# Optimization experiments

Measured on AMD Instinct MI355X. Metric: run time of the kernel, lower is better.

## Reference

```python
import jax, jax.numpy as jnp
import numpy as np

K = 3
STRIDE = 1
PAD = 1


def _conv(x, w, b):
    y = jax.lax.conv_general_dilated(
        x, w, window_strides=(STRIDE, STRIDE),
        padding=[(PAD, PAD), (PAD, PAD)],
        dimension_numbers=('NCHW', 'OIHW', 'NCHW'))
    return y + b[None, :, None, None]


def setup_inputs() -> dict:
    key = jax.random.key(0)
    ks = jax.random.split(key, 6)
    B, Cin, H, W = 4, 64, 128, 128
    Cout = 128
    x = jax.random.normal(ks[0], (B, Cin, H, W), dtype=jnp.float32)
    # small random offset/mask conv params (original inits to 0, which would be degenerate)
    w_off = jax.random.normal(ks[1], (2 * K * K, Cin, K, K), dtype=jnp.float32) * 0.01
    b_off = jax.random.normal(ks[2], (2 * K * K,), dtype=jnp.float32) * 0.1
    w_mask = jax.random.normal(ks[3], (K * K, Cin, K, K), dtype=jnp.float32) * 0.01
    b_mask = jnp.zeros((K * K,), dtype=jnp.float32)
    # kaiming_uniform(a=sqrt(5)) -> bound = 1/sqrt(fan_in)
    fan_in = Cin * K * K
    bound = 1.0 / np.sqrt(fan_in)
    weight = jax.random.uniform(ks[4], (Cout, Cin, K, K), dtype=jnp.float32,
                                minval=-bound, maxval=bound)
    return {"x": x, "w_off": w_off, "b_off": b_off,
            "w_mask": w_mask, "b_mask": b_mask, "weight": weight}


def _deform_conv(x, offset, mask, weight):
    B, C, H, W = x.shape
    O = weight.shape[0]
    KK = K * K
    Ho, Wo = offset.shape[2], offset.shape[3]
    # torchvision layout: offset[:, 2k] = dy_k, offset[:, 2k+1] = dx_k
    off = offset.reshape(B, KK, 2, Ho, Wo)
    dy, dx = off[:, :, 0], off[:, :, 1]  # [B,KK,Ho,Wo]

    ky, kx = jnp.meshgrid(jnp.arange(K), jnp.arange(K), indexing='ij')
    ky = ky.reshape(KK).astype(jnp.float32)
    kx = kx.reshape(KK).astype(jnp.float32)
    oy = jnp.arange(Ho, dtype=jnp.float32) * STRIDE - PAD
    ox = jnp.arange(Wo, dtype=jnp.float32) * STRIDE - PAD
    # sampling positions [B,KK,Ho,Wo]
    py = oy[None, None, :, None] + ky[None, :, None, None] + dy
    px = ox[None, None, None, :] + kx[None, :, None, None] + dx

    y0 = jnp.floor(py)
    x0 = jnp.floor(px)
    ly = py - y0
    lx = px - x0
    y0i = y0.astype(jnp.int32)
    x0i = x0.astype(jnp.int32)

    x_flat = x.reshape(B, C, H * W)
    gather = jax.vmap(lambda xf, idx: xf[:, idx])  # ([C,HW],[KK,Ho,Wo])->[C,KK,Ho,Wo]

    def corner(yi, xi, wgt):
        valid = ((yi >= 0) & (yi < H) & (xi >= 0) & (xi < W)).astype(x.dtype)
        yc = jnp.clip(yi, 0, H - 1)
        xc = jnp.clip(xi, 0, W - 1)
        g = gather(x_flat, yc * W + xc)  # [B,C,KK,Ho,Wo]
        return g * (wgt * valid)[:, None]

    sampled = (corner(y0i, x0i, (1 - ly) * (1 - lx))
               + corner(y0i, x0i + 1, (1 - ly) * lx)
               + corner(y0i + 1, x0i, ly * (1 - lx))
               + corner(y0i + 1, x0i + 1, ly * lx))  # [B,C,KK,Ho,Wo]

    sampled = sampled * mask[:, None]  # modulation, mask [B,KK,Ho,Wo]
    w = weight.reshape(O, C, KK)
    return jnp.einsum('bckhw,ock->bohw', sampled, w)


def reference(x, w_off, b_off, w_mask, b_mask, weight):
    offset = _conv(x, w_off, b_off)
    mask = jax.nn.sigmoid(_conv(x, w_mask, b_mask))
    return _deform_conv(x, offset, mask, weight)
```

## Files before the change

kernel.cpp:

```cpp
#include <hip/hip_runtime.h>
#include <math.h>

#define B 4
#define CIN 64
#define H 128
#define W 128
#define COUT 128
#define KK 9
#define HW (H*W)

#define WBF_COLS 640
#define WBF_SHORTS (COUT*WBF_COLS)
#define WCV_SHORTS (32*640)
#define LDK 168

typedef __attribute__((ext_vector_type(8))) short short8;
typedef __attribute__((ext_vector_type(4))) float f32x4;
typedef __attribute__((ext_vector_type(2))) float f32x2;
typedef f32x2 __attribute__((aligned(4))) f32x2a;

#define GLDS16(g, l) __builtin_amdgcn_global_load_lds(                        \
    (__attribute__((address_space(1))) void*)(g),                             \
    (__attribute__((address_space(3))) void*)(l), 16, 0, 0)

__device__ __forceinline__ unsigned short f2bf(float f) {
    unsigned int u = __float_as_uint(f);
    u += 0x7fffu + ((u >> 16) & 1u);
    return (unsigned short)(u >> 16);
}

__global__ void prep_all(const float* __restrict__ wgt,
                         const float* __restrict__ w_off, const float* __restrict__ b_off,
                         const float* __restrict__ w_mask, const float* __restrict__ b_mask,
                         short* __restrict__ wbf, short* __restrict__ wcv,
                         float* __restrict__ bcat)
{
    int idx = blockIdx.x * 256 + threadIdx.x;
    if (idx < WBF_SHORTS) {
        int o  = idx / WBF_COLS;
        int kp = idx % WBF_COLS;
        int cb = kp / 160, r = kp % 160;
        float v = 0.f;
        if (r < 144) {
            int tap = r >> 4;
            int c   = cb * 16 + (r & 15);
            v = wgt[(o * CIN + c) * KK + tap];
        }
        wbf[idx] = (short)f2bf(v);
    } else {
        int j = idx - WBF_SHORTS;
        if (j < WCV_SHORTS) {
            int f  = j / 640;
            int kp = j % 640;
            int cb = kp / 160, r = kp % 160;
            float v = 0.f;
            if (r < 144) {
                int tap = r >> 4;
                int c   = cb * 16 + (r & 15);
                if (f < 18)      v = w_off[(f * CIN + c) * 9 + tap];
                else if (f < 27) v = w_mask[((f - 18) * CIN + c) * 9 + tap];
            }
            wcv[j] = (short)f2bf(v);
        }
        if (blockIdx.x == WBF_SHORTS / 256 && threadIdx.x < 32) {
            int f = threadIdx.x;
            float bv = 0.f;
            if (f < 18) bv = b_off[f];
            else if (f < 27) bv = b_mask[f - 18];
            bcat[f] = bv;
        }
    }
}

__global__ __launch_bounds__(256, 2) void fused4_kernel(
    const float* __restrict__ x, const short* __restrict__ wcv,
    const short* __restrict__ wbf, const float* __restrict__ bcat,
    float* __restrict__ out)
{
    const int bid = blockIdx.x;
    const int T = (bid & 7) * 128 + (bid >> 3);
    const int wo0 = (T & 1) * 64;
    const int ho  = (T >> 1) & 127;
    const int b   = T >> 8;
    const int tid  = threadIdx.x;
    const int lane = tid & 63;
    const int wv   = tid >> 6;
    const int oh   = (wv & 1) * 64;
    const int ph   = (wv >> 1) * 32;
    const int row16 = lane & 15, kq = lane >> 4;

    __shared__ __align__(16) float XW[3456];
    __shared__ __align__(16) short S[64 * LDK];
    float* offs_l = (float*)S;

    const float* xb = x + (size_t)b * CIN * HW;

    int stA_goff[4];
    #pragma unroll
    for (int t = 0; t < 4; ++t) {
        int idx = tid + t * 256;
        int ci = idx / 54, rem = idx % 54, row = rem / 18, q = rem % 18;
        int ys = min(max(ho - 1 + row, 0), H - 1);
        int g0 = wo0 - 4 + q * 4;
        int g0c = min(max(g0, 0), W - 4);
        stA_goff[t] = ci * HW + ys * W + g0c;
    }
    auto stageA = [&](int c) {
        const float* base = xb + (size_t)c * 16 * HW;
        #pragma unroll
        for (int t = 0; t < 4; ++t) {
            if (tid + t * 256 < 864) {
                GLDS16(base + stA_goff[t], &XW[(tid + t * 256) * 4]);
            }
        }
    };

    if (tid < 128) {
        short8 z = {0,0,0,0,0,0,0,0};
        *(short8*)&S[(tid >> 1) * LDK + 144 + (tid & 1) * 8] = z;
    }
    stageA(0);

    int bidx[3];
    #pragma unroll
    for (int j = 0; j < 3; ++j) {
        bidx[j] = -1;
        int s = tid + j * 256;
        if (s < 576) {
            int k = s >> 6, p = s & 63;
            int ky = k / 3, kx = k % 3;
            bool ok = ((unsigned)(ho - 1 + ky) < (unsigned)H)
                   && ((unsigned)(wo0 + p - 1 + kx) < (unsigned)W);
            if (ok) bidx[j] = ky * 72 + (p + 3 + kx);
        }
    }
    int stB_goff[4];
    #pragma unroll
    for (int t = 0; t < 4; ++t) {
        int idx = tid + t * 256;
        int ci = idx / 108, rem = idx % 108, row = rem / 18, q = rem % 18;
        int ys = min(max(ho - 2 + row, 0), H - 1);
        int g0 = wo0 - 4 + q * 4;
        int g0c = min(max(g0, 0), W - 4);
        stB_goff[t] = ci * HW + ys * W + g0c;
    }
    __syncthreads();

    f32x4 acc2[2];
    acc2[0] = (f32x4){0.f, 0.f, 0.f, 0.f};
    acc2[1] = (f32x4){0.f, 0.f, 0.f, 0.f};

    auto buildA = [&]() {
        #pragma unroll
        for (int j = 0; j < 3; ++j) {
            int s = tid + j * 256;
            if (s < 576) {
                int k = s >> 6, p = s & 63;
                #pragma unroll
                for (int h2 = 0; h2 < 2; ++h2) {
                    short8 sv = {0,0,0,0,0,0,0,0};
                    if (bidx[j] >= 0) {
                        #pragma unroll
                        for (int c8 = 0; c8 < 8; ++c8)
                            sv[c8] = (short)f2bf(XW[(h2 * 8 + c8) * 216 + bidx[j]]);
                    }
                    *(short8*)&S[p * LDK + k * 16 + h2 * 8] = sv;
                }
            }
        }
    };
    auto mfmaA = [&](int c) {
        __builtin_amdgcn_s_setprio(1);
        #pragma unroll
        for (int ks = 0; ks < 5; ++ks) {
            short8 a0 = *(const short8*)(wcv + (row16)      * 640 + c * 160 + ks * 32 + kq * 8);
            short8 a1 = *(const short8*)(wcv + (16 + row16) * 640 + c * 160 + ks * 32 + kq * 8);
            short8 bfr = *(const short8*)&S[(wv * 16 + row16) * LDK + ks * 32 + kq * 8];
            acc2[0] = __builtin_amdgcn_mfma_f32_16x16x32_bf16(a0, bfr, acc2[0], 0, 0, 0);
            acc2[1] = __builtin_amdgcn_mfma_f32_16x16x32_bf16(a1, bfr, acc2[1], 0, 0, 0);
        }
        __builtin_amdgcn_s_setprio(0);
    };

    buildA();
    __syncthreads();
    #pragma unroll 1
    for (int c = 0; c < 3; ++c) {
        stageA(c + 1);
        mfmaA(c);
        __syncthreads();
        buildA();
        __syncthreads();
    }
    mfmaA(3);
    __syncthreads();

    {
        const int pxl = wv * 16 + row16;
        #pragma unroll
        for (int of = 0; of < 2; ++of) {
            #pragma unroll
            for (int r = 0; r < 4; ++r) {
                int f = of * 16 + kq * 4 + r;
                if (f < 27) {
                    float v = acc2[of][r] + bcat[f];
                    if (f >= 18) v = 1.f / (1.f + expf(-v));
                    offs_l[f * 64 + pxl] = v;
                }
            }
        }
    }
    __syncthreads();

    auto stageB = [&](int h) {
        const float* base = xb + (size_t)h * 8 * HW;
        #pragma unroll
        for (int t = 0; t < 4; ++t) {
            if (tid + t * 256 < 864) {
                GLDS16(base + stB_goff[t], &XW[(tid + t * 256) * 4]);
            }
        }
    };

    stageB(0);

    int   moff[3][2];
    int   lidx0[3], lidx1[3];
    f32x2 wAB[3], wCD[3];
    #pragma unroll
    for (int j = 0; j < 3; ++j) {
        moff[j][0] = 0; moff[j][1] = 0;
        lidx0[j] = -1; lidx1[j] = 0;
        wAB[j] = (f32x2){0.f, 0.f}; wCD[j] = (f32x2){0.f, 0.f};
        int s = tid + j * 256;
        if (s < 576) {
            int k = s >> 6, p = s & 63;
            int wo = wo0 + p;
            int ky = k / 3, kx = k % 3;
            float dy = offs_l[(2 * k) * 64 + p];
            float dx = offs_l[(2 * k + 1) * 64 + p];
            float mk = offs_l[(18 + k) * 64 + p];
            float py  = (float)(ho - 1 + ky) + dy;
            float pxf = (float)(wo - 1 + kx) + dx;
            float fy = floorf(py), fx = floorf(pxf);
            float ly = py - fy, lx = pxf - fx;
            int y0 = (int)fy, x0 = (int)fx;
            int y1 = y0 + 1,  x1 = x0 + 1;
            bool vy0 = (y0 >= 0) && (y0 < H);
            bool vy1 = (y1 >= 0) && (y1 < H);
            bool vx0 = (x0 >= 0) && (x0 < W);
            bool vx1 = (x1 >= 0) && (x1 < W);
            float w0 = (vy0 && vx0) ? (1.f - ly) * (1.f - lx) * mk : 0.f;
            float w1 = (vy0 && vx1) ? (1.f - ly) * lx * mk : 0.f;
            float w2 = (vy1 && vx0) ? ly * (1.f - lx) * mk : 0.f;
            float w3 = (vy1 && vx1) ? ly * lx * mk : 0.f;
            int lc = min(max(x0, 0), W - 2);
            bool sel = (x0 == lc);
            int r0 = min(max(y0, 0), H - 1);
            int r1 = min(max(y1, 0), H - 1);
            moff[j][0] = (r0 * W + lc) * 4;
            moff[j][1] = (r1 * W + lc) * 4;
            wAB[j].x = sel ? w0 : w1;  wAB[j].y = sel ? w1 : w0;
            wCD[j].x = sel ? w2 : w3;  wCD[j].y = sel ? w3 : w2;
            int u0 = r0 - (ho - 2);
            int u1 = r1 - (ho - 2);
            int vvv = lc - (wo0 - 4);
            bool fastp = ((unsigned)u0 < 6u) && ((unsigned)u1 < 6u)
                       && ((unsigned)vvv < 71u);
            lidx1[j] = u1 * 72 + vvv;
            lidx0[j] = fastp ? (u0 * 72 + vvv) : -1;
        }
    }
    __syncthreads();

    if (tid < 128) {
        short8 z = {0,0,0,0,0,0,0,0};
        *(short8*)&S[(tid >> 1) * LDK + 144 + (tid & 1) * 8] = z;
    }

    f32x4 acc[4][2];
    #pragma unroll
    for (int i = 0; i < 4; ++i)
        #pragma unroll
        for (int j = 0; j < 2; ++j)
            acc[i][j] = (f32x4){0.f, 0.f, 0.f, 0.f};

    auto sampleB = [&](int h) {
        #pragma unroll
        for (int j = 0; j < 3; ++j) {
            int s = tid + j * 256;
            if (s < 576) {
                int k = s >> 6, p = s & 63;
                float va[8];
                f32x2 wab = wAB[j], wcd = wCD[j];
                if (lidx0[j] >= 0) {
                    int l0 = lidx0[j], l1 = lidx1[j];
                    #pragma unroll
                    for (int ci = 0; ci < 8; ++ci) {
                        const float* bp = &XW[ci * 432];
                        f32x2 A  = *(const f32x2a*)(bp + l0);
                        f32x2 Bv = *(const f32x2a*)(bp + l1);
                        f32x2 t = A * wab + Bv * wcd;
                        va[ci] = t.x + t.y;
                    }
                } else {
                    #pragma unroll
                    for (int ci = 0; ci < 8; ++ci) {
                        const char* pc = (const char*)(xb + (size_t)(h * 8 + ci) * HW);
                        f32x2 A  = *(const f32x2a*)(pc + moff[j][0]);
                        f32x2 Bv = *(const f32x2a*)(pc + moff[j][1]);
                        f32x2 t = A * wab + Bv * wcd;
                        va[ci] = t.x + t.y;
                    }
                }
                short8 sv;
                #pragma unroll
                for (int ci = 0; ci < 8; ++ci) sv[ci] = (short)f2bf(va[ci]);
                *(short8*)&S[p * LDK + k * 16 + (h & 1) * 8] = sv;
            }
        }
    };

    auto mfmaB = [&](int c) {
        __builtin_amdgcn_s_setprio(1);
        #pragma unroll
        for (int ks = 0; ks < 5; ++ks) {
            short8 a[4];
            #pragma unroll
            for (int of = 0; of < 4; ++of) {
                int o = oh + of * 16 + row16;
                a[of] = *(const short8*)(wbf + o * WBF_COLS + c * 160 + ks * 32 + kq * 8);
            }
            #pragma unroll
            for (int pf = 0; pf < 2; ++pf) {
                int p = ph + pf * 16 + row16;
                short8 bfr = *(const short8*)&S[p * LDK + ks * 32 + kq * 8];
                #pragma unroll
                for (int of = 0; of < 4; ++of)
                    acc[of][pf] = __builtin_amdgcn_mfma_f32_16x16x32_bf16(
                        a[of], bfr, acc[of][pf], 0, 0, 0);
            }
        }
        __builtin_amdgcn_s_setprio(0);
    };

    sampleB(0); __syncthreads();
    stageB(1); __syncthreads(); sampleB(1); __syncthreads();
    #pragma unroll 1
    for (int c = 0; c < 3; ++c) {
        stageB(2 * c + 2);
        mfmaB(c);
        __syncthreads();
        sampleB(2 * c + 2);
        __syncthreads();
        stageB(2 * c + 3);
        __syncthreads();
        sampleB(2 * c + 3);
        __syncthreads();
    }
    mfmaB(3);

    #pragma unroll
    for (int of = 0; of < 4; ++of) {
        #pragma unroll
        for (int r = 0; r < 4; ++r) {
            int o = oh + of * 16 + kq * 4 + r;
            float* orow = out + ((b * COUT + o) * H + ho) * W;
            #pragma unroll
            for (int pf = 0; pf < 2; ++pf) {
                int wo = wo0 + ph + pf * 16 + row16;
                orow[wo] = acc[of][pf][r];
            }
        }
    }
}

extern "C" void kernel_launch(void* const* d_in, const int* in_sizes, int n_in,
                              void* d_out, int out_size, void* d_ws, size_t ws_size,
                              hipStream_t stream)
{
    const float* x      = (const float*)d_in[0];
    const float* w_off  = (const float*)d_in[1];
    const float* b_off  = (const float*)d_in[2];
    const float* w_mask = (const float*)d_in[3];
    const float* b_mask = (const float*)d_in[4];
    const float* weight = (const float*)d_in[5];
    float* out   = (float*)d_out;

    float* bcat  = (float*)d_ws;
    short* wbf   = (short*)(bcat + 32);
    short* wcv   = wbf + WBF_SHORTS;

    prep_all<<<dim3((WBF_SHORTS + WCV_SHORTS) / 256), 256, 0, stream>>>(
        weight, w_off, b_off, w_mask, b_mask, wbf, wcv, bcat);
    fused4_kernel<<<dim3(1024), 256, 0, stream>>>(x, wcv, wbf, bcat, out);
}
```

Measured before the change: 81.65 us.

## Halve pixel tile to 32 per block to double grid and occupancy

Each block now covers 32 output pixels of a row instead of 64, so the grid doubles to 2048 blocks and launch bounds ask for 4 blocks per CU. Shared staging buffers, per-thread sampling state and accumulator arrays shrink, which lowers LDS and register use and allows more concurrent waves to hide gather and load latency. In exchange, the halo columns are re-staged more often relative to useful work, and each wave issues fewer MFMAs per weight fragment load, so weight reuse drops and global weight traffic rises.

Measured after the change: 126.8 us. +55.3%, slower.

```diff
diff --git a/kernel.cpp b/kernel.cpp
--- a/kernel.cpp
+++ b/kernel.cpp
@@ -72,34 +72,34 @@
     }
 }
 
-__global__ __launch_bounds__(256, 2) void fused4_kernel(
+__global__ __launch_bounds__(256, 4) void fused6_kernel(
     const float* __restrict__ x, const short* __restrict__ wcv,
     const short* __restrict__ wbf, const float* __restrict__ bcat,
     float* __restrict__ out)
 {
     const int bid = blockIdx.x;
-    const int T = (bid & 7) * 128 + (bid >> 3);
-    const int wo0 = (T & 1) * 64;
-    const int ho  = (T >> 1) & 127;
-    const int b   = T >> 8;
+    const int T = (bid & 7) * 256 + (bid >> 3);
+    const int wo0 = (T & 3) * 32;
+    const int ho  = (T >> 2) & 127;
+    const int b   = T >> 9;
     const int tid  = threadIdx.x;
     const int lane = tid & 63;
     const int wv   = tid >> 6;
-    const int oh   = (wv & 1) * 64;
-    const int ph   = (wv >> 1) * 32;
+    const int wlo  = wv & 1;
+    const int whi  = wv >> 1;
     const int row16 = lane & 15, kq = lane >> 4;
 
-    __shared__ __align__(16) float XW[3456];
-    __shared__ __align__(16) short S[64 * LDK];
+    __shared__ __align__(16) float XW[1920];
+    __shared__ __align__(16) short S[32 * LDK];
     float* offs_l = (float*)S;
 
     const float* xb = x + (size_t)b * CIN * HW;
 
-    int stA_goff[4];
-    #pragma unroll
-    for (int t = 0; t < 4; ++t) {
+    int stA_goff[2];
+    #pragma unroll
+    for (int t = 0; t < 2; ++t) {
         int idx = tid + t * 256;
-        int ci = idx / 54, rem = idx % 54, row = rem / 18, q = rem % 18;
+        int ci = idx / 30, rem = idx % 30, row = rem / 10, q = rem % 10;
         int ys = min(max(ho - 1 + row, 0), H - 1);
         int g0 = wo0 - 4 + q * 4;
         int g0c = min(max(g0, 0), W - 4);
@@ -108,37 +108,37 @@
     auto stageA = [&](int c) {
         const float* base = xb + (size_t)c * 16 * HW;
         #pragma unroll
-        for (int t = 0; t < 4; ++t) {
-            if (tid + t * 256 < 864) {
+        for (int t = 0; t < 2; ++t) {
+            if (tid + t * 256 < 480) {
                 GLDS16(base + stA_goff[t], &XW[(tid + t * 256) * 4]);
             }
         }
     };
 
-    if (tid < 128) {
+    if (tid < 64) {
         short8 z = {0,0,0,0,0,0,0,0};
         *(short8*)&S[(tid >> 1) * LDK + 144 + (tid & 1) * 8] = z;
     }
     stageA(0);
 
-    int bidx[3];
-    #pragma unroll
-    for (int j = 0; j < 3; ++j) {
+    int bidx[2];
+    #pragma unroll
+    for (int j = 0; j < 2; ++j) {
         bidx[j] = -1;
         int s = tid + j * 256;
-        if (s < 576) {
-            int k = s >> 6, p = s & 63;
+        if (s < 288) {
+            int k = s >> 5, p = s & 31;
             int ky = k / 3, kx = k % 3;
             bool ok = ((unsigned)(ho - 1 + ky) < (unsigned)H)
                    && ((unsigned)(wo0 + p - 1 + kx) < (unsigned)W);
-            if (ok) bidx[j] = ky * 72 + (p + 3 + kx);
-        }
-    }
-    int stB_goff[4];
-    #pragma unroll
-    for (int t = 0; t < 4; ++t) {
+            if (ok) bidx[j] = ky * 40 + (p + 3 + kx);
+        }
+    }
+    int stB_goff[2];
+    #pragma unroll
+    for (int t = 0; t < 2; ++t) {
         int idx = tid + t * 256;
-        int ci = idx / 108, rem = idx % 108, row = rem / 18, q = rem % 18;
+        int ci = idx / 60, rem = idx % 60, row = rem / 10, q = rem % 10;
         int ys = min(max(ho - 2 + row, 0), H - 1);
         int g0 = wo0 - 4 + q * 4;
         int g0c = min(max(g0, 0), W - 4);
@@ -146,23 +146,21 @@
     }
     __syncthreads();
 
-    f32x4 acc2[2];
-    acc2[0] = (f32x4){0.f, 0.f, 0.f, 0.f};
-    acc2[1] = (f32x4){0.f, 0.f, 0.f, 0.f};
+    f32x4 acc2 = (f32x4){0.f, 0.f, 0.f, 0.f};
 
     auto buildA = [&]() {
         #pragma unroll
-        for (int j = 0; j < 3; ++j) {
+        for (int j = 0; j < 2; ++j) {
             int s = tid + j * 256;
-            if (s < 576) {
-                int k = s >> 6, p = s & 63;
+            if (s < 288) {
+                int k = s >> 5, p = s & 31;
                 #pragma unroll
                 for (int h2 = 0; h2 < 2; ++h2) {
                     short8 sv = {0,0,0,0,0,0,0,0};
                     if (bidx[j] >= 0) {
                         #pragma unroll
                         for (int c8 = 0; c8 < 8; ++c8)
-                            sv[c8] = (short)f2bf(XW[(h2 * 8 + c8) * 216 + bidx[j]]);
+                            sv[c8] = (short)f2bf(XW[(h2 * 8 + c8) * 120 + bidx[j]]);
                     }
                     *(short8*)&S[p * LDK + k * 16 + h2 * 8] = sv;
                 }
@@ -173,11 +171,11 @@
         __builtin_amdgcn_s_setprio(1);
         #pragma unroll
         for (int ks = 0; ks < 5; ++ks) {
-            short8 a0 = *(const short8*)(wcv + (row16)      * 640 + c * 160 + ks * 32 + kq * 8);
-            short8 a1 = *(const short8*)(wcv + (16 + row16) * 640 + c * 160 + ks * 32 + kq * 8);
-            short8 bfr = *(const short8*)&S[(wv * 16 + row16) * LDK + ks * 32 + kq * 8];
-            acc2[0] = __builtin_amdgcn_mfma_f32_16x16x32_bf16(a0, bfr, acc2[0], 0, 0, 0);
-            acc2[1] = __builtin_amdgcn_mfma_f32_16x16x32_bf16(a1, bfr, acc2[1], 0, 0, 0);
+            short8 a = *(const short8*)(wcv + (wlo * 16 + row16) * 640
+                                        + c * 160 + ks * 32 + kq * 8);
+            short8 bfr = *(const short8*)&S[(whi * 16 + row16) * LDK
+                                            + ks * 32 + kq * 8];
+            acc2 = __builtin_amdgcn_mfma_f32_16x16x32_bf16(a, bfr, acc2, 0, 0, 0);
         }
         __builtin_amdgcn_s_setprio(0);
     };
@@ -196,17 +194,14 @@
     __syncthreads();
 
     {
-        const int pxl = wv * 16 + row16;
-        #pragma unroll
-        for (int of = 0; of < 2; ++of) {
-            #pragma unroll
-            for (int r = 0; r < 4; ++r) {
-                int f = of * 16 + kq * 4 + r;
-                if (f < 27) {
-                    float v = acc2[of][r] + bcat[f];
-                    if (f >= 18) v = 1.f / (1.f + expf(-v));
-                    offs_l[f * 64 + pxl] = v;
-                }
+        const int pxl = whi * 16 + row16;
+        #pragma unroll
+        for (int r = 0; r < 4; ++r) {
+            int f = wlo * 16 + kq * 4 + r;
+            if (f < 27) {
+                float v = acc2[r] + bcat[f];
+                if (f >= 18) v = 1.f / (1.f + expf(-v));
+                offs_l[f * 32 + pxl] = v;
             }
         }
     }
@@ -215,8 +210,8 @@
     auto stageB = [&](int h) {
         const float* base = xb + (size_t)h * 8 * HW;
         #pragma unroll
-        for (int t = 0; t < 4; ++t) {
-            if (tid + t * 256 < 864) {
+        for (int t = 0; t < 2; ++t) {
+            if (tid + t * 256 < 480) {
                 GLDS16(base + stB_goff[t], &XW[(tid + t * 256) * 4]);
             }
         }
@@ -224,22 +219,22 @@
 
     stageB(0);
 
-    int   moff[3][2];
-    int   lidx0[3], lidx1[3];
-    f32x2 wAB[3], wCD[3];
-    #pragma unroll
-    for (int j = 0; j < 3; ++j) {
+    int   moff[2][2];
+    int   lidx0[2], lidx1[2];
+    f32x2 wAB[2], wCD[2];
+    #pragma unroll
+    for (int j = 0; j < 2; ++j) {
         moff[j][0] = 0; moff[j][1] = 0;
         lidx0[j] = -1; lidx1[j] = 0;
         wAB[j] = (f32x2){0.f, 0.f}; wCD[j] = (f32x2){0.f, 0.f};
         int s = tid + j * 256;
-        if (s < 576) {
-            int k = s >> 6, p = s & 63;
+        if (s < 288) {
+            int k = s >> 5, p = s & 31;
             int wo = wo0 + p;
             int ky = k / 3, kx = k % 3;
-            float dy = offs_l[(2 * k) * 64 + p];
-            float dx = offs_l[(2 * k + 1) * 64 + p];
-            float mk = offs_l[(18 + k) * 64 + p];
+            float dy = offs_l[(2 * k) * 32 + p];
+            float dx = offs_l[(2 * k + 1) * 32 + p];
+            float mk = offs_l[(18 + k) * 32 + p];
             float py  = (float)(ho - 1 + ky) + dy;
             float pxf = (float)(wo - 1 + kx) + dx;
             float fy = floorf(py), fx = floorf(pxf);
@@ -266,38 +261,35 @@
             int u1 = r1 - (ho - 2);
             int vvv = lc - (wo0 - 4);
             bool fastp = ((unsigned)u0 < 6u) && ((unsigned)u1 < 6u)
-                       && ((unsigned)vvv < 71u);
-            lidx1[j] = u1 * 72 + vvv;
-            lidx0[j] = fastp ? (u0 * 72 + vvv) : -1;
-        }
-    }
-    __syncthreads();
-
-    if (tid < 128) {
+                       && ((unsigned)vvv < 39u);
+            lidx1[j] = u1 * 40 + vvv;
+            lidx0[j] = fastp ? (u0 * 40 + vvv) : -1;
+        }
+    }
+    __syncthreads();
+
+    if (tid < 64) {
         short8 z = {0,0,0,0,0,0,0,0};
         *(short8*)&S[(tid >> 1) * LDK + 144 + (tid & 1) * 8] = z;
     }
 
-    f32x4 acc[4][2];
-    #pragma unroll
-    for (int i = 0; i < 4; ++i)
-        #pragma unroll
-        for (int j = 0; j < 2; ++j)
-            acc[i][j] = (f32x4){0.f, 0.f, 0.f, 0.f};
+    f32x4 acc[4];
+    #pragma unroll
+    for (int i = 0; i < 4; ++i) acc[i] = (f32x4){0.f, 0.f, 0.f, 0.f};
 
     auto sampleB = [&](int h) {
         #pragma unroll
-        for (int j = 0; j < 3; ++j) {
+        for (int j = 0; j < 2; ++j) {
             int s = tid + j * 256;
-            if (s < 576) {
-                int k = s >> 6, p = s & 63;
+            if (s < 288) {
+                int k = s >> 5, p = s & 31;
                 float va[8];
                 f32x2 wab = wAB[j], wcd = wCD[j];
                 if (lidx0[j] >= 0) {
                     int l0 = lidx0[j], l1 = lidx1[j];
                     #pragma unroll
                     for (int ci = 0; ci < 8; ++ci) {
-                        const float* bp = &XW[ci * 432];
+                        const float* bp = &XW[ci * 240];
                         f32x2 A  = *(const f32x2a*)(bp + l0);
                         f32x2 Bv = *(const f32x2a*)(bp + l1);
                         f32x2 t = A * wab + Bv * wcd;
@@ -328,18 +320,15 @@
             short8 a[4];
             #pragma unroll
             for (int of = 0; of < 4; ++of) {
-                int o = oh + of * 16 + row16;
+                int o = wlo * 64 + of * 16 + row16;
                 a[of] = *(const short8*)(wbf + o * WBF_COLS + c * 160 + ks * 32 + kq * 8);
             }
+            short8 bfr = *(const short8*)&S[(whi * 16 + row16) * LDK
+                                            + ks * 32 + kq * 8];
             #pragma unroll
-            for (int pf = 0; pf < 2; ++pf) {
-                int p = ph + pf * 16 + row16;
-                short8 bfr = *(const short8*)&S[p * LDK + ks * 32 + kq * 8];
-                #pragma unroll
-                for (int of = 0; of < 4; ++of)
-                    acc[of][pf] = __builtin_amdgcn_mfma_f32_16x16x32_bf16(
-                        a[of], bfr, acc[of][pf], 0, 0, 0);
-            }
+            for (int of = 0; of < 4; ++of)
+                acc[of] = __builtin_amdgcn_mfma_f32_16x16x32_bf16(
+                    a[of], bfr, acc[of], 0, 0, 0);
         }
         __builtin_amdgcn_s_setprio(0);
     };
@@ -360,16 +349,14 @@
     }
     mfmaB(3);
 
-    #pragma unroll
-    for (int of = 0; of < 4; ++of) {
-        #pragma unroll
-        for (int r = 0; r < 4; ++r) {
-            int o = oh + of * 16 + kq * 4 + r;
-            float* orow = out + ((b * COUT + o) * H + ho) * W;
+    {
+        const int wo = wo0 + whi * 16 + row16;
+        #pragma unroll
+        for (int of = 0; of < 4; ++of) {
             #pragma unroll
-            for (int pf = 0; pf < 2; ++pf) {
-                int wo = wo0 + ph + pf * 16 + row16;
-                orow[wo] = acc[of][pf][r];
+            for (int r = 0; r < 4; ++r) {
+                int o = wlo * 64 + of * 16 + kq * 4 + r;
+                out[((b * COUT + o) * H + ho) * W + wo] = acc[of][r];
             }
         }
     }
@@ -393,5 +380,5 @@
 
     prep_all<<<dim3((WBF_SHORTS + WCV_SHORTS) / 256), 256, 0, stream>>>(
         weight, w_off, b_off, w_mask, b_mask, wbf, wcv, bcat);
-    fused4_kernel<<<dim3(1024), 256, 0, stream>>>(x, wcv, wbf, bcat, out);
+    fused6_kernel<<<dim3(2048), 256, 0, stream>>>(x, wcv, wbf, bcat, out);
 }
```
